# Performance work log

Hardware: AMD Instinct MI355X
Metric: run time of the kernel (lower is better)

## Reference

```python
import jax, jax.numpy as jnp
import numpy as np

H = 512
INPUT_DIM = 13
OUTPUT_DIM = 1
W_DIM = (INPUT_DIM + OUTPUT_DIM) * H  # 7168
R = 256
N = 2048
LOG_2PI = float(np.log(2.0 * np.pi))


def setup_inputs() -> dict:
    key = jax.random.key(0)
    k1, k2, k3 = jax.random.split(key, 3)
    x = jax.random.normal(k1, (N, INPUT_DIM), dtype=jnp.float32)
    y = jax.random.normal(k2, (N, OUTPUT_DIM), dtype=jnp.float32)
    w = jax.random.normal(k3, (R, W_DIM), dtype=jnp.float32)
    return {"x": x, "y": y, "w": w}


def reference(x, y, w):
    # Batched version of FFReLU.loglik: for each weight sample r,
    #   w1 = w[r, :H*13].reshape(H, 13); w2 = w[r, H*13:].reshape(1, H)
    #   mu = w2 @ relu(w1 @ x.T)            -> [1, N]
    #   logprob[r] = Normal(mu.T, 1).log_prob(y).T
    w1_dim = H * INPUT_DIM
    w1 = w[:, :w1_dim].reshape(R, H, INPUT_DIM)       # [R, H, 13]
    w2 = w[:, w1_dim:].reshape(R, H)                  # [R, H] (output_dim = 1)
    hidden = jax.nn.relu(jnp.einsum('rhi,ni->rnh', w1, x))  # [R, N, H]
    mu = jnp.einsum('rnh,rh->rn', hidden, w2)         # [R, N]
    resid = y[:, 0][None, :] - mu                     # [R, N]
    log_p = -0.5 * resid * resid - 0.5 * LOG_2PI      # Normal(mu, 1) log-prob
    return log_p
```

## Files before the change

kernel.cpp:

```cpp
#include <hip/hip_runtime.h>

#define HH 512
#define IND 13
#define NN 2048
#define RR 256
#define WDIM 7168
#define W1DIM 6656
#define NBLK 256
#define NTHREADS 256
#define XPK_BYTES (NN * 32 * 2)
#define NEG_HALF_LOG_2PI (-0.91893853320467274f)

typedef __attribute__((ext_vector_type(8))) short short8;
typedef __attribute__((ext_vector_type(4))) float f32x4;
typedef __attribute__((ext_vector_type(2))) float f32x2;

__device__ __forceinline__ short f2bf(float f) {
    unsigned u = __float_as_uint(f);
    u += 0x7fffu + ((u >> 16) & 1u);
    return (short)(u >> 16);
}


__global__ __launch_bounds__(NTHREADS)
void xprep_kernel(const float* __restrict__ x, short* __restrict__ xpk) {
    const int n = blockIdx.x * NTHREADS + threadIdx.x;
    const float* xp = x + (size_t)n * IND;
    short tmp[32];
#pragma unroll
    for (int i = 0; i < 13; ++i) {
        float v = xp[i];
        unsigned u = __float_as_uint(v);
        tmp[i] = (short)(u >> 16);
        float res = v - __uint_as_float(u & 0xffff0000u);
        tmp[16 + i] = (short)(__float_as_uint(res) >> 16);
    }
    tmp[13] = 0; tmp[14] = 0; tmp[15] = 0;
    tmp[29] = 0; tmp[30] = 0; tmp[31] = 0;
    short8* dst = (short8*)(xpk + (size_t)n * 32);
    dst[0] = *(short8*)&tmp[0];
    dst[1] = *(short8*)&tmp[8];
    dst[2] = *(short8*)&tmp[16];
    dst[3] = *(short8*)&tmp[24];
}

template <bool FROM_WS>
__global__ __launch_bounds__(NTHREADS, 3)
void ffrelu_mfma_kernel(const float* __restrict__ x,
                        const float* __restrict__ y,
                        const float* __restrict__ w,
                        const short* __restrict__ xpk,
                        float* __restrict__ out) {
    __shared__ short Als[HH * 16];
    __shared__ float w2s[HH];

    const int tid = threadIdx.x;
    const int r = blockIdx.x;
    const int wave = tid >> 6;
    const int lane = tid & 63;
    const int m = lane & 15;
    const int q = lane >> 4;

    const float* wr = w + (size_t)r * WDIM;

#pragma unroll
    for (int rr = 0; rr < 2; ++rr) {
        const int h = tid * 2 + rr;
        const float* p = wr + (size_t)h * IND;
        short tmp[16];
#pragma unroll
        for (int i = 0; i < 13; ++i) tmp[i] = f2bf(p[i]);
        tmp[13] = 0; tmp[14] = 0; tmp[15] = 0;
        *(short8*)&Als[h * 16]     = *(short8*)&tmp[0];
        *(short8*)&Als[h * 16 + 8] = *(short8*)&tmp[8];
    }
    w2s[tid]       = wr[W1DIM + tid];
    w2s[tid + 256] = wr[W1DIM + tid + 256];
    __syncthreads();

    const bool lo  = (q >= 2);
    const bool hi8 = (q & 1);
    const f32x2 zero2 = {0.0f, 0.0f};
    const f32x4 czero = {0.0f, 0.0f, 0.0f, 0.0f};

    const int nb = blockIdx.y * NBLK + wave * 64;
    short8 bfrag[4];
    if (FROM_WS) {
        const short* base = xpk + (size_t)(nb + m) * 32 + (lo ? 16 : 0) + (hi8 ? 8 : 0);
#pragma unroll
        for (int nt = 0; nt < 4; ++nt) {
            bfrag[nt] = *(const short8*)(base + nt * 16 * 32);
        }
    } else {
#pragma unroll
        for (int nt = 0; nt < 4; ++nt) {
            const float* xp = x + (size_t)(nb + nt * 16 + m) * IND;
            short hs[13], ls[13];
#pragma unroll
            for (int i = 0; i < 13; ++i) {
                float v = xp[i];
                unsigned u = __float_as_uint(v);
                hs[i] = (short)(u >> 16);
                float res = v - __uint_as_float(u & 0xffff0000u);
                ls[i] = (short)(__float_as_uint(res) >> 16);
            }
            short s[13];
#pragma unroll
            for (int i = 0; i < 13; ++i) s[i] = lo ? ls[i] : hs[i];
            short8 b;
            b[0] = hi8 ? s[8]     : s[0];
            b[1] = hi8 ? s[9]     : s[1];
            b[2] = hi8 ? s[10]    : s[2];
            b[3] = hi8 ? s[11]    : s[3];
            b[4] = hi8 ? s[12]    : s[4];
            b[5] = hi8 ? (short)0 : s[5];
            b[6] = hi8 ? (short)0 : s[6];
            b[7] = hi8 ? (short)0 : s[7];
            bfrag[nt] = b;
        }
    }

    f32x2 muv[4][2];
#pragma unroll
    for (int i = 0; i < 4; ++i) {
        muv[i][0] = zero2;
        muv[i][1] = zero2;
    }

#pragma unroll 2
    for (int t = 0; t < 32; ++t) {
        const short8 a = *(const short8*)&Als[(t * 16 + m) * 16 + (q & 1) * 8];
        const f32x4 wv = *(const f32x4*)&w2s[t * 16 + q * 4];
        const f32x2 wv01 = {wv[0], wv[1]};
        const f32x2 wv23 = {wv[2], wv[3]};
#pragma unroll
        for (int nt = 0; nt < 4; ++nt) {
            f32x4 c = __builtin_amdgcn_mfma_f32_16x16x32_bf16(a, bfrag[nt], czero, 0, 0, 0);
            f32x2 c01 = {c[0], c[1]};
            f32x2 c23 = {c[2], c[3]};
            c01 = __builtin_elementwise_max(c01, zero2);
            c23 = __builtin_elementwise_max(c23, zero2);
            muv[nt][0] += c01 * wv01;
            muv[nt][1] += c23 * wv23;
        }
    }

    float mu[4];
#pragma unroll
    for (int nt = 0; nt < 4; ++nt) {
        f32x2 p = muv[nt][0] + muv[nt][1];
        float v = p[0] + p[1];
        v += __shfl_xor(v, 16, 64);
        v += __shfl_xor(v, 32, 64);
        mu[nt] = v;
    }

    float mu0;
    if (q == 0)      mu0 = mu[0];
    else if (q == 1) mu0 = mu[1];
    else if (q == 2) mu0 = mu[2];
    else             mu0 = mu[3];

    const int n0 = nb + lane;
    float resid0 = y[n0] - mu0;
    out[(size_t)r * NN + n0] = fmaf(-0.5f * resid0, resid0, NEG_HALF_LOG_2PI);
}

extern "C" void kernel_launch(void* const* d_in, const int* in_sizes, int n_in,
                              void* d_out, int out_size, void* d_ws, size_t ws_size,
                              hipStream_t stream) {
    const float* x = (const float*)d_in[0];
    const float* y = (const float*)d_in[1];
    const float* w = (const float*)d_in[2];
    float* out = (float*)d_out;
    short* xpk = (short*)d_ws;

    dim3 grid(RR, NN / NBLK);
    dim3 block(NTHREADS);

    if (ws_size >= (size_t)XPK_BYTES) {
        xprep_kernel<<<NN / NTHREADS, NTHREADS, 0, stream>>>(x, xpk);
        ffrelu_mfma_kernel<true><<<grid, block, 0, stream>>>(x, y, w, xpk, out);
    } else {
        ffrelu_mfma_kernel<false><<<grid, block, 0, stream>>>(x, y, w, xpk, out);
    }
}
```

Measured before the change: 91.36 us.

## Pre-pack W1 to bf16 in a prep kernel and read fragments from global/L2

Adds a wprep kernel that converts each sample's W1 to padded bf16 and copies W2 into the workspace once. The main kernel then reads its A fragments and w2 values straight from global memory (expected to hit L2) instead of staging them in LDS. This removes the redundant per-block conversion, the LDS staging and the __syncthreads that were repeated across the 8 N-blocks of each r. In exchange it adds a kernel launch and extra workspace traffic, and the inner loop now depends on global-load latency. The old in-kernel path stays as a fallback when the workspace is too small.

```diff
diff --git a/kernel.cpp b/kernel.cpp
--- a/kernel.cpp
+++ b/kernel.cpp
@@ -9,6 +9,8 @@
 #define NBLK 256
 #define NTHREADS 256
 #define XPK_BYTES (NN * 32 * 2)
+#define WPK_SHORTS_PER_R 9216
+#define WPK_BYTES (RR * WPK_SHORTS_PER_R * 2)
 #define NEG_HALF_LOG_2PI (-0.91893853320467274f)
 
 typedef __attribute__((ext_vector_type(8))) short short8;
@@ -44,16 +46,33 @@
     dst[3] = *(short8*)&tmp[24];
 }
 
-template <bool FROM_WS>
-__global__ __launch_bounds__(NTHREADS, 3)
-void ffrelu_mfma_kernel(const float* __restrict__ x,
-                        const float* __restrict__ y,
-                        const float* __restrict__ w,
-                        const short* __restrict__ xpk,
-                        float* __restrict__ out) {
-    __shared__ short Als[HH * 16];
-    __shared__ float w2s[HH];
-
+__global__ __launch_bounds__(NTHREADS)
+void wprep_kernel(const float* __restrict__ w, short* __restrict__ wpk) {
+    const int r = blockIdx.x;
+    const int tid = threadIdx.x;
+    const float* wr = w + (size_t)r * WDIM;
+    short* dst = wpk + (size_t)r * WPK_SHORTS_PER_R;
+#pragma unroll
+    for (int rr = 0; rr < 2; ++rr) {
+        const int h = tid * 2 + rr;
+        const float* p = wr + (size_t)h * IND;
+        short tmp[16];
+#pragma unroll
+        for (int i = 0; i < 13; ++i) tmp[i] = f2bf(p[i]);
+        tmp[13] = 0; tmp[14] = 0; tmp[15] = 0;
+        *(short8*)&dst[h * 16]     = *(short8*)&tmp[0];
+        *(short8*)&dst[h * 16 + 8] = *(short8*)&tmp[8];
+    }
+    float* w2d = (float*)(dst + HH * 16);
+    w2d[tid]       = wr[W1DIM + tid];
+    w2d[tid + 256] = wr[W1DIM + tid + 256];
+}
+
+__global__ __launch_bounds__(NTHREADS)
+void ffrelu_l2_kernel(const float* __restrict__ y,
+                      const short* __restrict__ wpk,
+                      const short* __restrict__ xpk,
+                      float* __restrict__ out) {
     const int tid = threadIdx.x;
     const int r = blockIdx.x;
     const int wave = tid >> 6;
@@ -61,22 +80,8 @@
     const int m = lane & 15;
     const int q = lane >> 4;
 
-    const float* wr = w + (size_t)r * WDIM;
-
-#pragma unroll
-    for (int rr = 0; rr < 2; ++rr) {
-        const int h = tid * 2 + rr;
-        const float* p = wr + (size_t)h * IND;
-        short tmp[16];
-#pragma unroll
-        for (int i = 0; i < 13; ++i) tmp[i] = f2bf(p[i]);
-        tmp[13] = 0; tmp[14] = 0; tmp[15] = 0;
-        *(short8*)&Als[h * 16]     = *(short8*)&tmp[0];
-        *(short8*)&Als[h * 16 + 8] = *(short8*)&tmp[8];
-    }
-    w2s[tid]       = wr[W1DIM + tid];
-    w2s[tid + 256] = wr[W1DIM + tid + 256];
-    __syncthreads();
+    const short* wr1 = wpk + (size_t)r * WPK_SHORTS_PER_R;
+    const float* w2p = (const float*)(wr1 + HH * 16);
 
     const bool lo  = (q >= 2);
     const bool hi8 = (q & 1);
@@ -84,40 +89,11 @@
     const f32x4 czero = {0.0f, 0.0f, 0.0f, 0.0f};
 
     const int nb = blockIdx.y * NBLK + wave * 64;
+    const short* xbase = xpk + (size_t)(nb + m) * 32 + (lo ? 16 : 0) + (hi8 ? 8 : 0);
     short8 bfrag[4];
-    if (FROM_WS) {
-        const short* base = xpk + (size_t)(nb + m) * 32 + (lo ? 16 : 0) + (hi8 ? 8 : 0);
-#pragma unroll
-        for (int nt = 0; nt < 4; ++nt) {
-            bfrag[nt] = *(const short8*)(base + nt * 16 * 32);
-        }
-    } else {
-#pragma unroll
-        for (int nt = 0; nt < 4; ++nt) {
-            const float* xp = x + (size_t)(nb + nt * 16 + m) * IND;
-            short hs[13], ls[13];
-#pragma unroll
-            for (int i = 0; i < 13; ++i) {
-                float v = xp[i];
-                unsigned u = __float_as_uint(v);
-                hs[i] = (short)(u >> 16);
-                float res = v - __uint_as_float(u & 0xffff0000u);
-                ls[i] = (short)(__float_as_uint(res) >> 16);
-            }
-            short s[13];
-#pragma unroll
-            for (int i = 0; i < 13; ++i) s[i] = lo ? ls[i] : hs[i];
-            short8 b;
-            b[0] = hi8 ? s[8]     : s[0];
-            b[1] = hi8 ? s[9]     : s[1];
-            b[2] = hi8 ? s[10]    : s[2];
-            b[3] = hi8 ? s[11]    : s[3];
-            b[4] = hi8 ? s[12]    : s[4];
-            b[5] = hi8 ? (short)0 : s[5];
-            b[6] = hi8 ? (short)0 : s[6];
-            b[7] = hi8 ? (short)0 : s[7];
-            bfrag[nt] = b;
-        }
+#pragma unroll
+    for (int nt = 0; nt < 4; ++nt) {
+        bfrag[nt] = *(const short8*)(xbase + nt * 16 * 32);
     }
 
     f32x2 muv[4][2];
@@ -129,8 +105,8 @@
 
 #pragma unroll 2
     for (int t = 0; t < 32; ++t) {
-        const short8 a = *(const short8*)&Als[(t * 16 + m) * 16 + (q & 1) * 8];
-        const f32x4 wv = *(const f32x4*)&w2s[t * 16 + q * 4];
+        const short8 a = *(const short8*)&wr1[(t * 16 + m) * 16 + (q & 1) * 8];
+        const f32x4 wv = *(const f32x4*)&w2p[t * 16 + q * 4];
         const f32x2 wv01 = {wv[0], wv[1]};
         const f32x2 wv23 = {wv[2], wv[3]};
 #pragma unroll
@@ -166,6 +142,118 @@
     out[(size_t)r * NN + n0] = fmaf(-0.5f * resid0, resid0, NEG_HALF_LOG_2PI);
 }
 
+__global__ __launch_bounds__(NTHREADS, 3)
+void ffrelu_fallback_kernel(const float* __restrict__ x,
+                            const float* __restrict__ y,
+                            const float* __restrict__ w,
+                            float* __restrict__ out) {
+    __shared__ short Als[HH * 16];
+    __shared__ float w2s[HH];
+
+    const int tid = threadIdx.x;
+    const int r = blockIdx.x;
+    const int wave = tid >> 6;
+    const int lane = tid & 63;
+    const int m = lane & 15;
+    const int q = lane >> 4;
+
+    const float* wr = w + (size_t)r * WDIM;
+
+#pragma unroll
+    for (int rr = 0; rr < 2; ++rr) {
+        const int h = tid * 2 + rr;
+        const float* p = wr + (size_t)h * IND;
+        short tmp[16];
+#pragma unroll
+        for (int i = 0; i < 13; ++i) tmp[i] = f2bf(p[i]);
+        tmp[13] = 0; tmp[14] = 0; tmp[15] = 0;
+        *(short8*)&Als[h * 16]     = *(short8*)&tmp[0];
+        *(short8*)&Als[h * 16 + 8] = *(short8*)&tmp[8];
+    }
+    w2s[tid]       = wr[W1DIM + tid];
+    w2s[tid + 256] = wr[W1DIM + tid + 256];
+    __syncthreads();
+
+    const bool lo  = (q >= 2);
+    const bool hi8 = (q & 1);
+    const f32x2 zero2 = {0.0f, 0.0f};
+    const f32x4 czero = {0.0f, 0.0f, 0.0f, 0.0f};
+
+    const int nb = blockIdx.y * NBLK + wave * 64;
+    short8 bfrag[4];
+#pragma unroll
+    for (int nt = 0; nt < 4; ++nt) {
+        const float* xp = x + (size_t)(nb + nt * 16 + m) * IND;
+        short hs[13], ls[13];
+#pragma unroll
+        for (int i = 0; i < 13; ++i) {
+            float v = xp[i];
+            unsigned u = __float_as_uint(v);
+            hs[i] = (short)(u >> 16);
+            float res = v - __uint_as_float(u & 0xffff0000u);
+            ls[i] = (short)(__float_as_uint(res) >> 16);
+        }
+        short s[13];
+#pragma unroll
+        for (int i = 0; i < 13; ++i) s[i] = lo ? ls[i] : hs[i];
+        short8 b;
+        b[0] = hi8 ? s[8]     : s[0];
+        b[1] = hi8 ? s[9]     : s[1];
+        b[2] = hi8 ? s[10]    : s[2];
+        b[3] = hi8 ? s[11]    : s[3];
+        b[4] = hi8 ? s[12]    : s[4];
+        b[5] = hi8 ? (short)0 : s[5];
+        b[6] = hi8 ? (short)0 : s[6];
+        b[7] = hi8 ? (short)0 : s[7];
+        bfrag[nt] = b;
+    }
+
+    f32x2 muv[4][2];
+#pragma unroll
+    for (int i = 0; i < 4; ++i) {
+        muv[i][0] = zero2;
+        muv[i][1] = zero2;
+    }
+
+#pragma unroll 2
+    for (int t = 0; t < 32; ++t) {
+        const short8 a = *(const short8*)&Als[(t * 16 + m) * 16 + (q & 1) * 8];
+        const f32x4 wv = *(const f32x4*)&w2s[t * 16 + q * 4];
+        const f32x2 wv01 = {wv[0], wv[1]};
+        const f32x2 wv23 = {wv[2], wv[3]};
+#pragma unroll
+        for (int nt = 0; nt < 4; ++nt) {
+            f32x4 c = __builtin_amdgcn_mfma_f32_16x16x32_bf16(a, bfrag[nt], czero, 0, 0, 0);
+            f32x2 c01 = {c[0], c[1]};
+            f32x2 c23 = {c[2], c[3]};
+            c01 = __builtin_elementwise_max(c01, zero2);
+            c23 = __builtin_elementwise_max(c23, zero2);
+            muv[nt][0] += c01 * wv01;
+            muv[nt][1] += c23 * wv23;
+        }
+    }
+
+    float mu[4];
+#pragma unroll
+    for (int nt = 0; nt < 4; ++nt) {
+        f32x2 p = muv[nt][0] + muv[nt][1];
+        float v = p[0] + p[1];
+        v += __shfl_xor(v, 16, 64);
+        v += __shfl_xor(v, 32, 64);
+        mu[nt] = v;
+    }
+
+    float mu0;
+    if (q == 0)      mu0 = mu[0];
+    else if (q == 1) mu0 = mu[1];
+    else if (q == 2) mu0 = mu[2];
+    else             mu0 = mu[3];
+
+    const int n0 = nb + lane;
+    float resid0 = y[n0] - mu0;
+    out[(size_t)r * NN + n0] = fmaf(-0.5f * resid0, resid0, NEG_HALF_LOG_2PI);
+}
+
 extern "C" void kernel_launch(void* const* d_in, const int* in_sizes, int n_in,
                               void* d_out, int out_size, void* d_ws, size_t ws_size,
                               hipStream_t stream) {
@@ -173,15 +261,17 @@
     const float* y = (const float*)d_in[1];
     const float* w = (const float*)d_in[2];
     float* out = (float*)d_out;
-    short* xpk = (short*)d_ws;
 
     dim3 grid(RR, NN / NBLK);
     dim3 block(NTHREADS);
 
-    if (ws_size >= (size_t)XPK_BYTES) {
+    if (ws_size >= (size_t)(XPK_BYTES + WPK_BYTES)) {
+        short* xpk = (short*)d_ws;
+        short* wpk = (short*)((char*)d_ws + XPK_BYTES);
         xprep_kernel<<<NN / NTHREADS, NTHREADS, 0, stream>>>(x, xpk);
-        ffrelu_mfma_kernel<true><<<grid, block, 0, stream>>>(x, y, w, xpk, out);
+        wprep_kernel<<<RR, NTHREADS, 0, stream>>>(w, wpk);
+        ffrelu_l2_kernel<<<grid, block, 0, stream>>>(y, wpk, xpk, out);
     } else {
-        ffrelu_mfma_kernel<false><<<grid, block, 0, stream>>>(x, y, w, xpk, out);
-    }
-}
+        ffrelu_fallback_kernel<<<grid, block, 0, stream>>>(x, y, w, out);
+    }
+}
```

Result: slower. 101.3 us (+10.9%).
